# Optimization experiments

Hardware: AMD Instinct MI355X
Metric: run time of the kernel (lower is better)

Reference implementation:

```python
import jax, jax.numpy as jnp
import numpy as np

VW, VD, VH = 96, 96, 96  # voxel_width, voxel_depth, voxel_height


def _grid_points():
    # voxel centers mapped to [-1, 1]: (2*i + 1 - N) / N
    xp = (2.0 * jnp.arange(VW) + 1.0 - VW) / VW
    yp = (2.0 * jnp.arange(VD) + 1.0 - VD) / VD
    zp = (2.0 * jnp.arange(VH) + 1.0 - VH) / VH
    X, Y, Z = jnp.meshgrid(xp, yp, zp, indexing='ij')
    return jnp.stack([X.ravel(), Y.ravel(), Z.ravel()], axis=-1)  # (V, 3)


def setup_inputs() -> dict:
    key = jax.random.key(0)
    k1, k2 = jax.random.split(key)
    B, NV, NF = 8, 2048, 512
    vertices = jax.random.uniform(k1, (B, NV, 3), dtype=jnp.float32, minval=-1.0, maxval=1.0)
    facets = jax.random.randint(k2, (B, NF, 4), 0, NV, dtype=jnp.int64)
    return {"vertices": vertices, "facets": facets}


def reference(vertices, facets):
    # vertices: (B, NV, 3) float32; facets: (B, NF, 4) int indices into vertices
    B = vertices.shape[0]
    NF = facets.shape[1]
    # vertices_to_facets: per-batch gather -> (B, NF, 4, 3)
    fverts = jax.vmap(lambda v, f: v[f])(vertices, facets)
    P = _grid_points()                      # (V, 3) voxel centers
    V = P.shape[0]

    def step(idx_map, xs):
        fi, verts = xs                      # verts: (B, 4, 3)
        v3 = verts[:, 3]                    # (B, 3)
        # T[:, j] = verts[j] - verts[3]  (columns are tetra edges)
        T = jnp.swapaxes(verts[:, :3] - v3[:, None, :], 1, 2)  # (B, 3, 3)
        a, b, c = T[:, 0, 0], T[:, 0, 1], T[:, 0, 2]
        d, e, f = T[:, 1, 0], T[:, 1, 1], T[:, 1, 2]
        g, h, i = T[:, 2, 0], T[:, 2, 1], T[:, 2, 2]
        # adjugate of T (matches t_inv_* in the original)
        adj = jnp.stack([
            jnp.stack([e * i - f * h, c * h - b * i, b * f - c * e], axis=-1),
            jnp.stack([f * g - d * i, a * i - c * g, c * d - a * f], axis=-1),
            jnp.stack([d * h - e * g, b * g - a * h, a * e - b * d], axis=-1),
        ], axis=1)                          # (B, 3, 3)
        det = a * (e * i - f * h) - b * (d * i - f * g) + c * (d * h - e * g)  # (B,)
        dvec = P[None, :, :] - v3[:, None, :]                  # (B, V, 3)
        lam = jnp.einsum('brc,bvc->bvr', adj, dvec) / det[:, None, None]  # (B, V, 3)
        lam4 = 1.0 - lam.sum(axis=-1, keepdims=True)
        lams = jnp.concatenate([lam, lam4], axis=-1)           # (B, V, 4)
        # original skips when any lambda < 0 or > 1 (strict) -> inside is inclusive
        inside = jnp.all((lams >= 0.0) & (lams <= 1.0), axis=-1)  # (B, V)
        idx_map = jnp.where((idx_map < 0) & inside, fi, idx_map)
        return idx_map, None

    idx0 = jnp.full((B, V), -1, dtype=jnp.int32)
    xs = (jnp.arange(NF, dtype=jnp.int32), jnp.swapaxes(fverts, 0, 1))
    idx_map, _ = jax.lax.scan(step, idx0, xs)
    alpha = (idx_map >= 0).astype(jnp.float32).reshape(B, VW, VD, VH)
    return alpha
```

## Files before the change

### kernel.cpp

```cpp
#include <hip/hip_runtime.h>

#pragma clang fp contract(off)

#define VWD 96
#define NVERT 2048
#define NFAC 512
#define NBATCH 8
#define NSLAB 3456
#define RECF 16
#define CULC 22

#define CUL(c, b, f) cul[(size_t)(c) * (NBATCH * NFAC) + (size_t)(b) * NFAC + (f)]

__global__ __launch_bounds__(512) void precompute_kernel(
    const float* __restrict__ vertices,
    const int*   __restrict__ facets,
    float*       __restrict__ cul,
    float*       __restrict__ body)
{
    __shared__ unsigned skey[NFAC];
    const int b = blockIdx.x;
    const int j = threadIdx.x;
    const float* vb = vertices + (size_t)b * NVERT * 3;

    int4 fi = ((const int4*)facets)[b * NFAC + j];
    float x0 = vb[3*fi.x+0], y0 = vb[3*fi.x+1], z0 = vb[3*fi.x+2];
    float x1 = vb[3*fi.y+0], y1 = vb[3*fi.y+1], z1 = vb[3*fi.y+2];
    float x2 = vb[3*fi.z+0], y2 = vb[3*fi.z+1], z2 = vb[3*fi.z+2];
    float x3 = vb[3*fi.w+0], y3 = vb[3*fi.w+1], z3 = vb[3*fi.w+2];
    float a  = x0-x3, bb = x1-x3, c  = x2-x3;
    float d  = y0-y3, e  = y1-y3, f  = y2-y3;
    float g  = z0-z3, h  = z1-z3, ii = z2-z3;
    float A00 = e*ii - f*h,  A01 = c*h  - bb*ii, A02 = bb*f - c*e;
    float A10 = f*g  - d*ii, A11 = a*ii - c*g,   A12 = c*d  - a*f;
    float A20 = d*h  - e*g,  A21 = bb*g - a*h,   A22 = a*e  - bb*d;
    float det = a*(e*ii - f*h) - bb*(d*ii - f*g) + c*(d*h - e*g);
    if (det < 0.0f) {
        det = -det;
        A00 = -A00; A01 = -A01; A02 = -A02;
        A10 = -A10; A11 = -A11; A12 = -A12;
        A20 = -A20; A21 = -A21; A22 = -A22;
    }
    unsigned myk = ~__float_as_uint(det);
    skey[j] = myk;
    __syncthreads();

    int rank = 0;
    const uint4* sk4 = (const uint4*)skey;
    for (int k0 = 0; k0 < NFAC; k0 += 4) {
        uint4 kk = sk4[k0 >> 2];
        rank += (kk.x < myk) + ((kk.x == myk) & (k0 + 0 < j));
        rank += (kk.y < myk) + ((kk.y == myk) & (k0 + 1 < j));
        rank += (kk.z < myk) + ((kk.z == myk) & (k0 + 2 < j));
        rank += (kk.w < myk) + ((kk.w == myk) & (k0 + 3 < j));
    }

    CUL(0, b, rank) = fminf(fminf(x0,x1),fminf(x2,x3)) - 1e-4f;
    CUL(1, b, rank) = fminf(fminf(y0,y1),fminf(y2,y3)) - 1e-4f;
    CUL(2, b, rank) = fminf(fminf(z0,z1),fminf(z2,z3)) - 1e-4f;
    CUL(3, b, rank) = fmaxf(fmaxf(x0,x1),fmaxf(x2,x3)) + 1e-4f;
    CUL(4, b, rank) = fmaxf(fmaxf(y0,y1),fmaxf(y2,y3)) + 1e-4f;
    CUL(5, b, rank) = fmaxf(fmaxf(z0,z1),fmaxf(z2,z3)) + 1e-4f;

    const float HX = 7.0f/96.0f, HZ = 3.0f/96.0f;
    auto plane = [&](float pax, float pay, float paz,
                     float pbx, float pby, float pbz,
                     float pcx, float pcy, float pcz,
                     float pox, float poy, float poz, int base) {
        float e1x = pbx-pax, e1y = pby-pay, e1z = pbz-paz;
        float e2x = pcx-pax, e2y = pcy-pay, e2z = pcz-paz;
        float nx = e1y*e2z - e1z*e2y;
        float ny = e1z*e2x - e1x*e2z;
        float nz = e1x*e2y - e1y*e2x;
        float sdot = nx*(pox-pax) + ny*(poy-pay) + nz*(poz-paz);
        if (sdot > 0.0f) { nx=-nx; ny=-ny; nz=-nz; sdot=-sdot; }
        float dpl = nx*pax + ny*pay + nz*paz;
        float n1s = fabsf(nx)+fabsf(ny)+fabsf(nz);
        float M = 1e-4f*(-sdot) + 1e-4f*n1s + 1e-4f;
        float rhs = dpl + M + (fabsf(nx)*HX + fabsf(ny)*HX + fabsf(nz)*HZ);
        CUL(base+0, b, rank) = nx;
        CUL(base+1, b, rank) = ny;
        CUL(base+2, b, rank) = nz;
        CUL(base+3, b, rank) = rhs;
    };
    plane(x1,y1,z1, x2,y2,z2, x3,y3,z3, x0,y0,z0, 6);
    plane(x0,y0,z0, x2,y2,z2, x3,y3,z3, x1,y1,z1, 10);
    plane(x0,y0,z0, x1,y1,z1, x3,y3,z3, x2,y2,z2, 14);
    plane(x0,y0,z0, x1,y1,z1, x2,y2,z2, x3,y3,z3, 18);

    float* bo = body + ((size_t)b * NFAC + rank) * RECF;
    bo[0]  = det; bo[1]  = x3;  bo[2]  = y3;  bo[3]  = z3;
    bo[4]  = A00; bo[5]  = A01; bo[6]  = A02; bo[7]  = A10;
    bo[8]  = A11; bo[9]  = A12; bo[10] = A20; bo[11] = A21;
    bo[12] = A22;
    bo[13] = det * (1.0f - 1e-5f) - 1e-25f;
    bo[14] = det * (1.0f + 1e-5f) + 1e-25f;
    bo[15] = 0.0f;
}

__global__ __launch_bounds__(512) void mask_kernel(
    const float* __restrict__ cul,
    unsigned long long* __restrict__ masks)
{
    const int col = blockIdx.x;
    const int b   = blockIdx.y;
    const int f   = threadIdx.x;
    const int w   = threadIdx.x >> 6;
    float bminx=CUL(0,b,f), bminy=CUL(1,b,f), bminz=CUL(2,b,f);
    float bmaxx=CUL(3,b,f), bmaxy=CUL(4,b,f), bmaxz=CUL(5,b,f);
    float n0x=CUL(6,b,f),  n0y=CUL(7,b,f),  n0z=CUL(8,b,f),  r0=CUL(9,b,f);
    float n1x=CUL(10,b,f), n1y=CUL(11,b,f), n1z=CUL(12,b,f), r1=CUL(13,b,f);
    float n2x=CUL(14,b,f), n2y=CUL(15,b,f), n2z=CUL(16,b,f), r2=CUL(17,b,f);
    float n3x=CUL(18,b,f), n3y=CUL(19,b,f), n3z=CUL(20,b,f), r3=CUL(21,b,f);

    const int sx = col / 12, sy = col % 12;
    const float cx = (float)(16*sx + 8 - VWD) / 96.0f;
    const float cy = (float)(16*sy + 8 - VWD) / 96.0f;
    const float colminx = (float)(16*sx + 1  - VWD) / 96.0f;
    const float colmaxx = (float)(16*sx + 15 - VWD) / 96.0f;
    const float colminy = (float)(16*sy + 1  - VWD) / 96.0f;
    const float colmaxy = (float)(16*sy + 15 - VWD) / 96.0f;
    const bool ovxy = (bminx <= colmaxx) & (bmaxx >= colminx) &
                      (bminy <= colmaxy) & (bmaxy >= colminy);

    const float cz0   = (float)(4 - VWD) / 96.0f;
    const float stepc = 8.0f / 96.0f;
    float d0 = n0x*cx + n0y*cy + n0z*cz0 - r0;  float s0 = n0z*stepc;
    float d1 = n1x*cx + n1y*cy + n1z*cz0 - r1;  float s1 = n1z*stepc;
    float d2 = n2x*cx + n2y*cy + n2z*cz0 - r2;  float s2 = n2z*stepc;
    float d3 = n3x*cx + n3y*cy + n3z*cz0 - r3;  float s3 = n3z*stepc;
    float zlo = (float)(1 - VWD) / 96.0f;
    float zhi = (float)(7 - VWD) / 96.0f;

    unsigned long long* mp = masks + ((size_t)b * NSLAB + (size_t)col * 24) * 8 + w;
#pragma unroll 4
    for (int sz = 0; sz < 24; ++sz) {
        bool ov = ovxy & (bminz <= zhi) & (bmaxz >= zlo) &
                  (d0 <= 0.0f) & (d1 <= 0.0f) & (d2 <= 0.0f) & (d3 <= 0.0f);
        unsigned long long bal = __ballot((int)ov);
        if ((threadIdx.x & 63) == 0) mp[(size_t)sz * 8] = bal;
        d0 += s0; d1 += s1; d2 += s2; d3 += s3;
        zlo += stepc; zhi += stepc;
    }
}

__global__ __launch_bounds__(128) void voxelize_kernel(
    const float*              __restrict__ body,
    const unsigned long long* __restrict__ masks,
    float*                    __restrict__ out)
{
    const int b    = blockIdx.y;
    const int wave = threadIdx.x >> 6;
    const int lane = threadIdx.x & 63;
    const int slab = blockIdx.x * 2 + wave;
    const int sz = slab % 24;
    const int sy = (slab / 24) % 12;
    const int sx = slab / 288;
    const int ix  = sx*8 + (lane >> 3);
    const int iy  = sy*8 + (lane & 7);
    const int iz0 = sz*4;

    const float px  = (float)(2*ix + 1 - VWD) / 96.0f;
    const float py  = (float)(2*iy + 1 - VWD) / 96.0f;
    const float pz0 = (float)(2*(iz0+0) + 1 - VWD) / 96.0f;
    const float pz1 = (float)(2*(iz0+1) + 1 - VWD) / 96.0f;
    const float pz2 = (float)(2*(iz0+2) + 1 - VWD) / 96.0f;
    const float pz3 = (float)(2*(iz0+3) + 1 - VWD) / 96.0f;

    const unsigned long long* mp = masks + ((size_t)b * NSLAB + slab) * 8;
    const float* bb = body + (size_t)b * NFAC * RECF;

    unsigned fnd = 0u;
    for (int w = 0; w < 8; ++w) {
        unsigned long long m = mp[w];
        while (m) {
            int bit = __builtin_ctzll(m);
            m &= m - 1;
            int f = __builtin_amdgcn_readfirstlane(w * 64 + bit);
            const float* bo = bb + f * RECF;
            float det = bo[0], v3x = bo[1], v3y = bo[2], v3z = bo[3];
            float A00 = bo[4],  A01 = bo[5],  A02 = bo[6],  A10 = bo[7];
            float A11 = bo[8],  A12 = bo[9],  A20 = bo[10], A21 = bo[11];
            float A22 = bo[12], dhi = bo[13], mhi = bo[14];
            float dx = px - v3x, dy = py - v3y;
            float p0 = A00*dx + A01*dy;
            float p1 = A10*dx + A11*dy;
            float p2 = A20*dx + A21*dy;
            float dzk0 = pz0 - v3z, dzk1 = pz1 - v3z;
            float dzk2 = pz2 - v3z, dzk3 = pz3 - v3z;
            unsigned need = 0u;
#pragma unroll
            for (int k = 0; k < 4; ++k) {
                float dzk = (k == 0) ? dzk0 : (k == 1) ? dzk1
                          : (k == 2) ? dzk2 : dzk3;
                float n0 = p0 + A02*dzk;
                float n1 = p1 + A12*dzk;
                float n2 = p2 + A22*dzk;
                float sm = (n0 + n1) + n2;
                float mn = fminf(fminf(n0, n1), n2);
                bool ge0 = (mn >= 0.0f);
                bool def = ge0 & (sm <= dhi);
                bool may = ge0 & (sm <= mhi);
                if (may & !def & !((fnd >> k) & 1u)) need |= (1u << k);
                if (def) fnd |= (1u << k);
            }
            if (__any(need != 0u)) {
#pragma unroll
                for (int k = 0; k < 4; ++k) {
                    float dzk = (k == 0) ? dzk0 : (k == 1) ? dzk1
                              : (k == 2) ? dzk2 : dzk3;
                    float n0 = p0 + A02*dzk;
                    float n1 = p1 + A12*dzk;
                    float n2 = p2 + A22*dzk;
                    float l0 = n0 / det;
                    float l1 = n1 / det;
                    float l2 = n2 / det;
                    float l3 = 1.0f - ((l0 + l1) + l2);
                    bool inside = (l0 >= 0.0f) & (l0 <= 1.0f) &
                                  (l1 >= 0.0f) & (l1 <= 1.0f) &
                                  (l2 >= 0.0f) & (l2 <= 1.0f) &
                                  (l3 >= 0.0f) & (l3 <= 1.0f);
                    if (((need >> k) & 1u) & inside) fnd |= (1u << k);
                }
            }
            if (__all(fnd == 15u)) goto done;
        }
    }
done:
    float4 v;
    v.x = (fnd & 1u) ? 1.0f : 0.0f;
    v.y = (fnd & 2u) ? 1.0f : 0.0f;
    v.z = (fnd & 4u) ? 1.0f : 0.0f;
    v.w = (fnd & 8u) ? 1.0f : 0.0f;
    *(float4*)&out[(size_t)b*(VWD*VWD*VWD) + (size_t)ix*(VWD*VWD) + iy*VWD + iz0] = v;
}

extern "C" void kernel_launch(void* const* d_in, const int* in_sizes, int n_in,
                              void* d_out, int out_size, void* d_ws, size_t ws_size,
                              hipStream_t stream) {
    const float* vertices = (const float*)d_in[0];
    const int*   facets   = (const int*)d_in[1];
    float*       out      = (float*)d_out;

    float* cul  = (float*)d_ws;
    float* body = (float*)((char*)d_ws + (size_t)CULC * NBATCH * NFAC * 4);
    unsigned long long* msk =
        (unsigned long long*)((char*)d_ws +
                              (size_t)(CULC + RECF) * NBATCH * NFAC * 4);

    precompute_kernel<<<NBATCH, 512, 0, stream>>>(vertices, facets, cul, body);
    mask_kernel<<<dim3(144, NBATCH), 512, 0, stream>>>(cul, msk);
    dim3 grid(NSLAB / 2, NBATCH);
    voxelize_kernel<<<grid, 128, 0, stream>>>(body, msk, out);
}
```

Measured before the change: 144.4 us.

## Add edge-cross-product separating axis tests to tetra-slab culling masks

```diff
diff --git a/kernel.cpp b/kernel.cpp
--- a/kernel.cpp
+++ b/kernel.cpp
@@ -8,7 +8,7 @@
 #define NBATCH 8
 #define NSLAB 3456
 #define RECF 16
-#define CULC 22
+#define CULC 94
 
 #define CUL(c, b, f) cul[(size_t)(c) * (NBATCH * NFAC) + (size_t)(b) * NFAC + (f)]
 
@@ -88,6 +88,37 @@
     plane(x0,y0,z0, x1,y1,z1, x3,y3,z3, x2,y2,z2, 14);
     plane(x0,y0,z0, x1,y1,z1, x2,y2,z2, x3,y3,z3, 18);
 
+    auto axis = [&](float c1, float c2,
+                    float t0, float t1, float t2, float t3,
+                    float r, int base) {
+        float tmin = fminf(fminf(t0,t1), fminf(t2,t3));
+        float tmax = fmaxf(fmaxf(t0,t1), fmaxf(t2,t3));
+        float M = 1e-4f*(fabsf(c1)+fabsf(c2)) + 1e-5f;
+        CUL(base+0, b, rank) = c1;
+        CUL(base+1, b, rank) = c2;
+        CUL(base+2, b, rank) = tmin - r - M;
+        CUL(base+3, b, rank) = tmax + r + M;
+    };
+    auto edge = [&](float xA, float yA, float zA,
+                    float xB, float yB, float zB, int base) {
+        float ex = xB-xA, ey = yB-yA, ez = zB-zA;
+        axis(ez, -ey,
+             ez*y0 - ey*z0, ez*y1 - ey*z1, ez*y2 - ey*z2, ez*y3 - ey*z3,
+             fabsf(ez)*HX + fabsf(ey)*HZ, base+0);
+        axis(-ez, ex,
+             ex*z0 - ez*x0, ex*z1 - ez*x1, ex*z2 - ez*x2, ex*z3 - ez*x3,
+             fabsf(ez)*HX + fabsf(ex)*HZ, base+4);
+        axis(ey, -ex,
+             ey*x0 - ex*y0, ey*x1 - ex*y1, ey*x2 - ex*y2, ey*x3 - ex*y3,
+             fabsf(ey)*HX + fabsf(ex)*HX, base+8);
+    };
+    edge(x0,y0,z0, x1,y1,z1, 22 + 0*12);
+    edge(x0,y0,z0, x2,y2,z2, 22 + 1*12);
+    edge(x0,y0,z0, x3,y3,z3, 22 + 2*12);
+    edge(x1,y1,z1, x2,y2,z2, 22 + 3*12);
+    edge(x1,y1,z1, x3,y3,z3, 22 + 4*12);
+    edge(x2,y2,z2, x3,y3,z3, 22 + 5*12);
+
     float* bo = body + ((size_t)b * NFAC + rank) * RECF;
     bo[0]  = det; bo[1]  = x3;  bo[2]  = y3;  bo[3]  = z3;
     bo[4]  = A00; bo[5]  = A01; bo[6]  = A02; bo[7]  = A10;
@@ -120,8 +151,18 @@
     const float colmaxx = (float)(16*sx + 15 - VWD) / 96.0f;
     const float colminy = (float)(16*sy + 1  - VWD) / 96.0f;
     const float colmaxy = (float)(16*sy + 15 - VWD) / 96.0f;
-    const bool ovxy = (bminx <= colmaxx) & (bmaxx >= colminx) &
-                      (bminy <= colmaxy) & (bmaxy >= colminy);
+    bool ovxy = (bminx <= colmaxx) & (bmaxx >= colminx) &
+                (bminy <= colmaxy) & (bmaxy >= colminy);
+
+#pragma unroll
+    for (int e = 0; e < 6; ++e) {
+        float c1 = CUL(22 + e*12 + 8,  b, f);
+        float c2 = CUL(22 + e*12 + 9,  b, f);
+        float lo = CUL(22 + e*12 + 10, b, f);
+        float hi = CUL(22 + e*12 + 11, b, f);
+        float dd = c1*cx + c2*cy;
+        ovxy = ovxy & (dd >= lo) & (dd <= hi);
+    }
 
     const float cz0   = (float)(4 - VWD) / 96.0f;
     const float stepc = 8.0f / 96.0f;
@@ -129,6 +170,25 @@
     float d1 = n1x*cx + n1y*cy + n1z*cz0 - r1;  float s1 = n1z*stepc;
     float d2 = n2x*cx + n2y*cy + n2z*cz0 - r2;  float s2 = n2z*stepc;
     float d3 = n3x*cx + n3y*cy + n3z*cz0 - r3;  float s3 = n3z*stepc;
+
+    float eu[12], ev[12], es[12];
+#pragma unroll
+    for (int e = 0; e < 6; ++e) {
+#pragma unroll
+        for (int t = 0; t < 2; ++t) {
+            int base = 22 + e*12 + t*4;
+            float c1 = CUL(base+0, b, f);
+            float c2 = CUL(base+1, b, f);
+            float lo = CUL(base+2, b, f);
+            float hi = CUL(base+3, b, f);
+            float dd = c1 * (t == 0 ? cy : cx) + c2 * cz0;
+            int idx = e*2 + t;
+            eu[idx] = dd - lo;
+            ev[idx] = hi - dd;
+            es[idx] = c2 * stepc;
+        }
+    }
+
     float zlo = (float)(1 - VWD) / 96.0f;
     float zhi = (float)(7 - VWD) / 96.0f;
 
@@ -137,9 +197,14 @@
     for (int sz = 0; sz < 24; ++sz) {
         bool ov = ovxy & (bminz <= zhi) & (bmaxz >= zlo) &
                   (d0 <= 0.0f) & (d1 <= 0.0f) & (d2 <= 0.0f) & (d3 <= 0.0f);
+#pragma unroll
+        for (int q = 0; q < 12; ++q)
+            ov = ov & (eu[q] >= 0.0f) & (ev[q] >= 0.0f);
         unsigned long long bal = __ballot((int)ov);
         if ((threadIdx.x & 63) == 0) mp[(size_t)sz * 8] = bal;
         d0 += s0; d1 += s1; d2 += s2; d3 += s3;
+#pragma unroll
+        for (int q = 0; q < 12; ++q) { eu[q] += es[q]; ev[q] -= es[q]; }
         zlo += stepc; zhi += stepc;
     }
 }
```

Measured after the change: 165.6 us. +14.7%, slower.
